# Kernel tuning notes

Hardware: AMD Instinct MI355X
Metric: run time of the kernel (lower is better)

## Reference

```python
import jax, jax.numpy as jnp
import numpy as np

N, TX, TZ, DX, DZ, DATT, DOUT = 8, 2048, 2048, 1024, 1024, 1024, 1024


def setup_inputs() -> dict:
    key = jax.random.key(0)
    ks = jax.random.split(key, 8)
    s = 0.02
    x = jax.random.normal(ks[0], (N, TX, DX), dtype=jnp.float32)
    z = jax.random.normal(ks[1], (N, TZ, DZ), dtype=jnp.float32)
    Wq = jax.random.normal(ks[2], (DX, DATT), dtype=jnp.float32) * s
    bq = jnp.zeros((DATT,), dtype=jnp.float32)
    Wk = jax.random.normal(ks[3], (DZ, DATT), dtype=jnp.float32) * s
    bk = jnp.zeros((DATT,), dtype=jnp.float32)
    Wv = jax.random.normal(ks[4], (DZ, DOUT), dtype=jnp.float32) * s
    bv = jnp.zeros((DOUT,), dtype=jnp.float32)
    # fixed boolean mask [Tx, Tz]; causal lower-triangular so no row is fully masked
    mask = jnp.tril(jnp.ones((TX, TZ), dtype=bool))
    return {"x": x, "z": z, "Wq": Wq, "bq": bq, "Wk": Wk, "bk": bk,
            "Wv": Wv, "bv": bv, "mask": mask}


def reference(x, z, Wq, bq, Wk, bk, Wv, bv, mask):
    Datt = Wq.shape[1]
    Q = x @ Wq + bq                      # [N, Tx, Datt]
    K = z @ Wk + bk                      # [N, Tz, Datt]
    V = z @ Wv + bv                      # [N, Tz, Dout]
    S = jnp.einsum('bxd,bzd->bxz', Q, K)  # [N, Tx, Tz]
    S = jnp.where(mask[None, :, :], S, -jnp.inf)
    A = jax.nn.softmax(S / jnp.sqrt(jnp.float32(Datt)), axis=-1)
    y = jnp.einsum('bxz,bzo->bxo', A, V)  # [N, Tx, Dout]
    return y
```

## Files before the change

### kernel.cpp

```cpp
#include <hip/hip_runtime.h>

typedef _Float16 f16;
typedef _Float16 f16x8 __attribute__((ext_vector_type(8)));
typedef _Float16 f16x4 __attribute__((ext_vector_type(4)));
typedef float    f32x4 __attribute__((ext_vector_type(4)));

constexpr int NB   = 8;
constexpr int T    = 2048;
constexpr int D    = 1024;
constexpr int NTRI = 136;

__device__ __forceinline__ void load_lds16(const f16* g, f16* l) {
    __builtin_amdgcn_global_load_lds(
        (const __attribute__((address_space(1))) void*)g,
        (__attribute__((address_space(3))) void*)l, 16, 0, 0);
}

__global__ __launch_bounds__(256) void cast_transpose_w(
    const float* __restrict__ W0, const float* __restrict__ W1,
    const float* __restrict__ W2, f16* __restrict__ Wt)
{
    __shared__ f16 tile[32][33];
    const int which = blockIdx.z;
    const float* W = which == 0 ? W0 : (which == 1 ? W1 : W2);
    f16* dst = Wt + (size_t)which * D * D;
    const int c0 = blockIdx.x * 32, r0 = blockIdx.y * 32;
    const int tx = threadIdx.x & 31, ty = threadIdx.x >> 5;
    #pragma unroll
    for (int i = 0; i < 32; i += 8)
        tile[ty + i][tx] = (f16)W[(size_t)(r0 + ty + i) * D + c0 + tx];
    __syncthreads();
    #pragma unroll
    for (int i = 0; i < 32; i += 8)
        dst[(size_t)(c0 + ty + i) * D + r0 + tx] = tile[tx][ty + i];
}

__global__ __launch_bounds__(256) void cast_xz(
    const float* __restrict__ x, const float* __restrict__ z,
    f16* __restrict__ xh, f16* __restrict__ zh)
{
    const float* src = blockIdx.y ? z : x;
    f16* dst = blockIdx.y ? zh : xh;
    const size_t i = ((size_t)blockIdx.x * 256 + threadIdx.x) * 4;
    const float4 v = *(const float4*)(src + i);
    f16x4 u = { (f16)v.x, (f16)v.y, (f16)v.z, (f16)v.w };
    *(f16x4*)(dst + i) = u;
}

template<int MODE>
__global__ __launch_bounds__(256) void gemm_nt(
    const f16* __restrict__ Ag_, const f16* __restrict__ Bg_,
    void* __restrict__ Cg_, void* __restrict__ Cg2_,
    const float* __restrict__ bias, const float* __restrict__ bias2,
    float* __restrict__ rsum)
{
    __shared__ f16 As[2 * 128 * 32];
    __shared__ f16 Bs[2 * 128 * 32];

    int bx, by;
    const int bz = blockIdx.z;
    if (MODE == 1) {
        const int idx = blockIdx.x;
        by = (int)((sqrtf(8.0f * idx + 1.0f) - 1.0f) * 0.5f);
        while ((by + 1) * (by + 2) / 2 <= idx) ++by;
        while (by * (by + 1) / 2 > idx) --by;
        bx = idx - by * (by + 1) / 2;
    } else if (MODE == 2) {
        bx = blockIdx.x; by = 15 - blockIdx.y;
    } else {
        bx = blockIdx.x; by = blockIdx.y;
    }

    const size_t bm0 = (size_t)by * 128, bn0 = (size_t)bx * 128;
    const f16* Abase; const f16* Bbase;
    int lda, ldb, K;
    if (MODE == 0 || MODE == 4) {
        Abase = Ag_ + bm0 * D;                       lda = D;
        Bbase = Bg_ + bn0 * D;                       ldb = D; K = D;
    } else if (MODE == 1) {
        Abase = Ag_ + (size_t)bz * T * D + bm0 * D;  lda = D;
        Bbase = Bg_ + (size_t)bz * T * D + bn0 * D;  ldb = D; K = D;
    } else {
        Abase = Ag_ + ((size_t)bz * NTRI + (size_t)by * (by + 1) / 2) * 16384;
        lda = 128;
        Bbase = Bg_ + (size_t)bz * D * T + bn0 * T;  ldb = T;
        K = (by + 1) * 128;
    }

    const int t    = threadIdx.x;
    const int lane = t & 63, wave = t >> 6;
    const int wr   = (wave >> 1) * 64, wc = (wave & 1) * 64;
    const int fr   = lane & 15, fo = (lane >> 4) * 8;
    const int srow = t >> 2;
    const int scol = (t & 3) * 8;
    const int wub  = (t & 192) * 8;

    f32x4 acc[4][4] = {};

    for (int k0 = 0; k0 < K; k0 += 64) {
        #pragma unroll
        for (int p = 0; p < 2; ++p) {
            const int k = k0 + p * 32;
            const f16* Ak;
            if (MODE == 2) Ak = Abase + (size_t)(k >> 7) * 16384 + (k & 127);
            else           Ak = Abase + k;
            #pragma unroll
            for (int it = 0; it < 2; ++it)
                load_lds16(Ak + (size_t)(it * 64 + srow) * lda + scol,
                           As + p * 4096 + it * 2048 + wub);
            #pragma unroll
            for (int it = 0; it < 2; ++it)
                load_lds16(Bbase + k + (size_t)(it * 64 + srow) * ldb + scol,
                           Bs + p * 4096 + it * 2048 + wub);
        }
        __syncthreads();

        #pragma unroll
        for (int p = 0; p < 2; ++p) {
            f16x8 av[4], bv[4];
            #pragma unroll
            for (int i = 0; i < 4; ++i)
                av[i] = *(const f16x8*)&As[p * 4096 + (wr + i * 16 + fr) * 32 + fo];
            #pragma unroll
            for (int j = 0; j < 4; ++j)
                bv[j] = *(const f16x8*)&Bs[p * 4096 + (wc + j * 16 + fr) * 32 + fo];
            #pragma unroll
            for (int i = 0; i < 4; ++i)
                #pragma unroll
                for (int j = 0; j < 4; ++j)
                    acc[i][j] = __builtin_amdgcn_mfma_f32_16x16x32_f16(av[i], bv[j], acc[i][j], 0, 0, 0);
        }
        __syncthreads();
    }

    const int cr = (lane >> 4) * 4, cc = lane & 15;
    if (MODE == 0) {
        f16* Cp = (f16*)Cg_;
        #pragma unroll
        for (int j = 0; j < 4; ++j) {
            const int col = (int)bn0 + wc + j * 16 + cc;
            const float bb = bias[col];
            #pragma unroll
            for (int i = 0; i < 4; ++i)
                #pragma unroll
                for (int g = 0; g < 4; ++g)
                    Cp[(bm0 + wr + i * 16 + cr + g) * D + col] = (f16)(acc[i][j][g] + bb);
        }
    } else if (MODE == 4) {
        if (bx < 8) {
            f16* Cp = (f16*)Cg_;
            #pragma unroll
            for (int j = 0; j < 4; ++j) {
                const int col = (int)bn0 + wc + j * 16 + cc;
                const float bb = bias[col];
                #pragma unroll
                for (int i = 0; i < 4; ++i)
                    #pragma unroll
                    for (int g = 0; g < 4; ++g)
                        Cp[(bm0 + wr + i * 16 + cr + g) * D + col] = (f16)(acc[i][j][g] + bb);
            }
        } else {
            f16* Vt = (f16*)Cg2_;
            const int b  = (int)(bm0 >> 11);
            const int r0 = (int)(bm0 & 2047);
            #pragma unroll
            for (int j = 0; j < 4; ++j) {
                const int colv = (int)bn0 - 1024 + wc + j * 16 + cc;
                const float bb = bias2[colv];
                #pragma unroll
                for (int i = 0; i < 4; ++i) {
                    f16x4 pk = { (f16)(acc[i][j][0] + bb), (f16)(acc[i][j][1] + bb),
                                 (f16)(acc[i][j][2] + bb), (f16)(acc[i][j][3] + bb) };
                    *(f16x4*)&Vt[(size_t)b * D * T + (size_t)colv * T + r0 + wr + i * 16 + cr] = pk;
                }
            }
        }
    } else if (MODE == 1) {
        f16* Cp = (f16*)Cg_ + ((size_t)bz * NTRI + (size_t)by * (by + 1) / 2 + bx) * 16384;
        float* rs = rsum + (size_t)bz * T + bm0;
        float rowsum[4][4] = {};
        #pragma unroll
        for (int i = 0; i < 4; ++i)
            #pragma unroll
            for (int j = 0; j < 4; ++j)
                #pragma unroll
                for (int g = 0; g < 4; ++g) {
                    const int lr = wr + i * 16 + cr + g, lc = wc + j * 16 + cc;
                    const int r = (int)bm0 + lr, c = (int)bn0 + lc;
                    const float p = (c > r) ? 0.0f : __expf(acc[i][j][g] * 0.03125f);
                    Cp[lr * 128 + lc] = (f16)p;
                    rowsum[i][g] += p;
                }
        #pragma unroll
        for (int i = 0; i < 4; ++i)
            #pragma unroll
            for (int g = 0; g < 4; ++g) {
                float s = rowsum[i][g];
                s += __shfl_xor(s, 1, 64);
                s += __shfl_xor(s, 2, 64);
                s += __shfl_xor(s, 4, 64);
                s += __shfl_xor(s, 8, 64);
                if (cc == 0) atomicAdd(&rs[wr + i * 16 + cr + g], s);
            }
    } else {
        float* Cp = (float*)Cg_ + (size_t)bz * T * D;
        const float* rs = rsum + (size_t)bz * T;
        #pragma unroll
        for (int i = 0; i < 4; ++i) {
            const int r4 = (int)bm0 + wr + i * 16 + cr;
            float rinv[4];
            #pragma unroll
            for (int g = 0; g < 4; ++g) rinv[g] = 1.0f / rs[r4 + g];
            #pragma unroll
            for (int j = 0; j < 4; ++j)
                #pragma unroll
                for (int g = 0; g < 4; ++g)
                    Cp[(size_t)(r4 + g) * D + bn0 + wc + j * 16 + cc] = acc[i][j][g] * rinv[g];
        }
    }
}

extern "C" void kernel_launch(void* const* d_in, const int* in_sizes, int n_in,
                              void* d_out, int out_size, void* d_ws, size_t ws_size,
                              hipStream_t stream)
{
    const float* x  = (const float*)d_in[0];
    const float* z  = (const float*)d_in[1];
    const float* Wq = (const float*)d_in[2];
    const float* bq = (const float*)d_in[3];
    const float* Wk = (const float*)d_in[4];
    const float* bk = (const float*)d_in[5];
    const float* Wv = (const float*)d_in[6];
    const float* bv = (const float*)d_in[7];
    float* out = (float*)d_out;

    char* ws = (char*)d_ws;
    f16*   Wt   = (f16*)(ws);
    f16*   xh   = (f16*)(ws + 6291456ull);
    f16*   zh   = (f16*)(ws + 39845888ull);
    f16*   Qh   = (f16*)(ws + 73400320ull);
    f16*   Kh   = (f16*)(ws + 106954752ull);
    f16*   Vt   = (f16*)(ws + 140509184ull);
    f16*   SA   = (f16*)(ws + 174063616ull);
    float* rsum = (float*)(ws + 209715200ull);

    hipMemsetAsync(rsum, 0, (size_t)NB * T * sizeof(float), stream);
    cast_transpose_w<<<dim3(32, 32, 3), 256, 0, stream>>>(Wq, Wk, Wv, Wt);
    cast_xz<<<dim3(16384, 2, 1), 256, 0, stream>>>(x, z, xh, zh);
    gemm_nt<0><<<dim3(8, 128, 1), 256, 0, stream>>>(xh, Wt, Qh, nullptr, bq, nullptr, nullptr);
    gemm_nt<4><<<dim3(16, 128, 1), 256, 0, stream>>>(zh, Wt + 1048576, Kh, Vt, bk, bv, nullptr);
    gemm_nt<1><<<dim3(136, 1, 8), 256, 0, stream>>>(Qh, Kh, SA, nullptr, nullptr, nullptr, rsum);
    gemm_nt<2><<<dim3(8, 16, 8), 256, 0, stream>>>(SA, Vt, out, nullptr, nullptr, nullptr, rsum);
}
```

Before: 500.2 us.

## Fuse fp32-to-fp16 input cast into a single QKV projection GEMM

Removes the separate cast_xz kernel and the fp16 copies of x and z. A new gemm_qkv kernel loads fp32 x/z tiles straight into XOR-swizzled LDS and converts them to fp16 in registers before the MFMA, which saves a full read-write pass over the activations. It also merges the Q and K/V projection launches into one 24-column grid. The attention GEMMs drop from a 64-wide double-buffered K step to a 32-wide single buffer, which halves LDS use but doubles the number of barriers. The cast now uses round-toward-zero, a small change in numerics.

```diff
diff --git a/kernel.cpp b/kernel.cpp
--- a/kernel.cpp
+++ b/kernel.cpp
@@ -3,6 +3,7 @@
 typedef _Float16 f16;
 typedef _Float16 f16x8 __attribute__((ext_vector_type(8)));
 typedef _Float16 f16x4 __attribute__((ext_vector_type(4)));
+typedef __fp16   h16x2 __attribute__((ext_vector_type(2)));
 typedef float    f32x4 __attribute__((ext_vector_type(4)));
 
 constexpr int NB   = 8;
@@ -10,7 +11,7 @@
 constexpr int D    = 1024;
 constexpr int NTRI = 136;
 
-__device__ __forceinline__ void load_lds16(const f16* g, f16* l) {
+__device__ __forceinline__ void load_lds16(const void* g, void* l) {
     __builtin_amdgcn_global_load_lds(
         (const __attribute__((address_space(1))) void*)g,
         (__attribute__((address_space(3))) void*)l, 16, 0, 0);
@@ -35,27 +36,107 @@
         dst[(size_t)(c0 + ty + i) * D + r0 + tx] = tile[tx][ty + i];
 }
 
-__global__ __launch_bounds__(256) void cast_xz(
-    const float* __restrict__ x, const float* __restrict__ z,
-    f16* __restrict__ xh, f16* __restrict__ zh)
-{
-    const float* src = blockIdx.y ? z : x;
-    f16* dst = blockIdx.y ? zh : xh;
-    const size_t i = ((size_t)blockIdx.x * 256 + threadIdx.x) * 4;
-    const float4 v = *(const float4*)(src + i);
-    f16x4 u = { (f16)v.x, (f16)v.y, (f16)v.z, (f16)v.w };
-    *(f16x4*)(dst + i) = u;
+__global__ __launch_bounds__(256) void gemm_qkv(
+    const float* __restrict__ xg, const float* __restrict__ zg,
+    const f16* __restrict__ Wt,
+    f16* __restrict__ Qh, f16* __restrict__ Kh, f16* __restrict__ Vt,
+    const float* __restrict__ bq, const float* __restrict__ bk,
+    const float* __restrict__ bv)
+{
+    __shared__ __align__(16) float As32[128 * 32];
+    __shared__ __align__(16) f16   Bs[128 * 32];
+
+    const int bx = blockIdx.x, by = blockIdx.y;
+    const size_t bm0 = (size_t)by * 128, bn0 = (size_t)bx * 128;
+    const float* Ag = (bx < 8) ? xg : zg;
+    const f16*   Bg = Wt + bn0 * D;
+
+    const int t    = threadIdx.x;
+    const int lane = t & 63, wave = t >> 6;
+    const int wr   = (wave >> 1) * 64, wc = (wave & 1) * 64;
+    const int fr   = lane & 15, fo = (lane >> 4) * 8;
+    const int srow16 = t >> 2, scol16 = (t & 3) * 8, wub16 = (t & 192) * 8;
+    const int arow = (lane >> 3);
+    const int acol = (((lane & 7) ^ arow) << 2);
+
+    f32x4 acc[4][4] = {};
+
+    for (int k0 = 0; k0 < D; k0 += 32) {
+        #pragma unroll
+        for (int it = 0; it < 4; ++it)
+            load_lds16(Ag + (bm0 + it * 32 + wave * 8 + arow) * D + k0 + acol,
+                       As32 + it * 1024 + wave * 256);
+        #pragma unroll
+        for (int it = 0; it < 2; ++it)
+            load_lds16(Bg + k0 + (size_t)(it * 64 + srow16) * D + scol16,
+                       Bs + it * 2048 + wub16);
+        __syncthreads();
+
+        f16x8 av[4], bvv[4];
+        #pragma unroll
+        for (int i = 0; i < 4; ++i) {
+            const int rA = wr + i * 16 + fr;
+            const int sw = rA & 7;
+            const float* Ra = As32 + rA * 32;
+            const float4 lo = *(const float4*)(Ra + ((((fo >> 2) + 0) ^ sw) << 2));
+            const float4 hi = *(const float4*)(Ra + ((((fo >> 2) + 1) ^ sw) << 2));
+            union { f16x8 v; h16x2 h[4]; } u;
+            u.h[0] = __builtin_amdgcn_cvt_pkrtz(lo.x, lo.y);
+            u.h[1] = __builtin_amdgcn_cvt_pkrtz(lo.z, lo.w);
+            u.h[2] = __builtin_amdgcn_cvt_pkrtz(hi.x, hi.y);
+            u.h[3] = __builtin_amdgcn_cvt_pkrtz(hi.z, hi.w);
+            av[i] = u.v;
+        }
+        #pragma unroll
+        for (int j = 0; j < 4; ++j)
+            bvv[j] = *(const f16x8*)&Bs[(wc + j * 16 + fr) * 32 + fo];
+        #pragma unroll
+        for (int i = 0; i < 4; ++i)
+            #pragma unroll
+            for (int j = 0; j < 4; ++j)
+                acc[i][j] = __builtin_amdgcn_mfma_f32_16x16x32_f16(av[i], bvv[j], acc[i][j], 0, 0, 0);
+        __syncthreads();
+    }
+
+    const int cr = (lane >> 4) * 4, cc = lane & 15;
+    const int grp = bx >> 3;
+    if (grp < 2) {
+        f16* Cp = grp == 0 ? Qh : Kh;
+        const float* bias = grp == 0 ? bq : bk;
+        #pragma unroll
+        for (int j = 0; j < 4; ++j) {
+            const int col = (int)bn0 - grp * 1024 + wc + j * 16 + cc;
+            const float bb = bias[col];
+            #pragma unroll
+            for (int i = 0; i < 4; ++i)
+                #pragma unroll
+                for (int g = 0; g < 4; ++g)
+                    Cp[(bm0 + wr + i * 16 + cr + g) * D + col] = (f16)(acc[i][j][g] + bb);
+        }
+    } else {
+        const int b  = (int)(bm0 >> 11);
+        const int r0 = (int)(bm0 & 2047);
+        #pragma unroll
+        for (int j = 0; j < 4; ++j) {
+            const int colv = (int)bn0 - 2048 + wc + j * 16 + cc;
+            const float bb = bv[colv];
+            #pragma unroll
+            for (int i = 0; i < 4; ++i) {
+                f16x4 pk = { (f16)(acc[i][j][0] + bb), (f16)(acc[i][j][1] + bb),
+                             (f16)(acc[i][j][2] + bb), (f16)(acc[i][j][3] + bb) };
+                *(f16x4*)&Vt[(size_t)b * D * T + (size_t)colv * T + r0 + wr + i * 16 + cr] = pk;
+            }
+        }
+    }
 }
 
 template<int MODE>
-__global__ __launch_bounds__(256) void gemm_nt(
+__global__ __launch_bounds__(256) void gemm_attn(
     const f16* __restrict__ Ag_, const f16* __restrict__ Bg_,
-    void* __restrict__ Cg_, void* __restrict__ Cg2_,
-    const float* __restrict__ bias, const float* __restrict__ bias2,
-    float* __restrict__ rsum)
-{
-    __shared__ f16 As[2 * 128 * 32];
-    __shared__ f16 Bs[2 * 128 * 32];
+    void* __restrict__ Cg_, float* __restrict__ rsum)
+{
+    __shared__ __align__(16) f16 As[128 * 32];
+    __shared__ __align__(16) f16 Bs[128 * 32];
 
     int bx, by;
     const int bz = blockIdx.z;
@@ -65,19 +146,14 @@
         while ((by + 1) * (by + 2) / 2 <= idx) ++by;
         while (by * (by + 1) / 2 > idx) --by;
         bx = idx - by * (by + 1) / 2;
-    } else if (MODE == 2) {
+    } else {
         bx = blockIdx.x; by = 15 - blockIdx.y;
-    } else {
-        bx = blockIdx.x; by = blockIdx.y;
     }
 
     const size_t bm0 = (size_t)by * 128, bn0 = (size_t)bx * 128;
     const f16* Abase; const f16* Bbase;
     int lda, ldb, K;
-    if (MODE == 0 || MODE == 4) {
-        Abase = Ag_ + bm0 * D;                       lda = D;
-        Bbase = Bg_ + bn0 * D;                       ldb = D; K = D;
-    } else if (MODE == 1) {
+    if (MODE == 1) {
         Abase = Ag_ + (size_t)bz * T * D + bm0 * D;  lda = D;
         Bbase = Bg_ + (size_t)bz * T * D + bn0 * D;  ldb = D; K = D;
     } else {
@@ -91,91 +167,41 @@
     const int lane = t & 63, wave = t >> 6;
     const int wr   = (wave >> 1) * 64, wc = (wave & 1) * 64;
     const int fr   = lane & 15, fo = (lane >> 4) * 8;
-    const int srow = t >> 2;
-    const int scol = (t & 3) * 8;
-    const int wub  = (t & 192) * 8;
+    const int srow = t >> 2, scol = (t & 3) * 8, wub = (t & 192) * 8;
 
     f32x4 acc[4][4] = {};
 
-    for (int k0 = 0; k0 < K; k0 += 64) {
-        #pragma unroll
-        for (int p = 0; p < 2; ++p) {
-            const int k = k0 + p * 32;
-            const f16* Ak;
-            if (MODE == 2) Ak = Abase + (size_t)(k >> 7) * 16384 + (k & 127);
-            else           Ak = Abase + k;
-            #pragma unroll
-            for (int it = 0; it < 2; ++it)
-                load_lds16(Ak + (size_t)(it * 64 + srow) * lda + scol,
-                           As + p * 4096 + it * 2048 + wub);
-            #pragma unroll
-            for (int it = 0; it < 2; ++it)
-                load_lds16(Bbase + k + (size_t)(it * 64 + srow) * ldb + scol,
-                           Bs + p * 4096 + it * 2048 + wub);
-        }
-        __syncthreads();
-
-        #pragma unroll
-        for (int p = 0; p < 2; ++p) {
-            f16x8 av[4], bv[4];
-            #pragma unroll
-            for (int i = 0; i < 4; ++i)
-                av[i] = *(const f16x8*)&As[p * 4096 + (wr + i * 16 + fr) * 32 + fo];
-            #pragma unroll
-            for (int j = 0; j < 4; ++j)
-                bv[j] = *(const f16x8*)&Bs[p * 4096 + (wc + j * 16 + fr) * 32 + fo];
-            #pragma unroll
-            for (int i = 0; i < 4; ++i)
-                #pragma unroll
-                for (int j = 0; j < 4; ++j)
-                    acc[i][j] = __builtin_amdgcn_mfma_f32_16x16x32_f16(av[i], bv[j], acc[i][j], 0, 0, 0);
-        }
+    for (int k0 = 0; k0 < K; k0 += 32) {
+        const f16* Ak;
+        if (MODE == 2) Ak = Abase + (size_t)(k0 >> 7) * 16384 + (k0 & 127);
+        else           Ak = Abase + k0;
+        #pragma unroll
+        for (int it = 0; it < 2; ++it)
+            load_lds16(Ak + (size_t)(it * 64 + srow) * lda + scol,
+                       As + it * 2048 + wub);
+        #pragma unroll
+        for (int it = 0; it < 2; ++it)
+            load_lds16(Bbase + k0 + (size_t)(it * 64 + srow) * ldb + scol,
+                       Bs + it * 2048 + wub);
+        __syncthreads();
+
+        f16x8 av[4], bvv[4];
+        #pragma unroll
+        for (int i = 0; i < 4; ++i)
+            av[i] = *(const f16x8*)&As[(wr + i * 16 + fr) * 32 + fo];
+        #pragma unroll
+        for (int j = 0; j < 4; ++j)
+            bvv[j] = *(const f16x8*)&Bs[(wc + j * 16 + fr) * 32 + fo];
+        #pragma unroll
+        for (int i = 0; i < 4; ++i)
+            #pragma unroll
+            for (int j = 0; j < 4; ++j)
+                acc[i][j] = __builtin_amdgcn_mfma_f32_16x16x32_f16(av[i], bvv[j], acc[i][j], 0, 0, 0);
         __syncthreads();
     }
 
     const int cr = (lane >> 4) * 4, cc = lane & 15;
-    if (MODE == 0) {
-        f16* Cp = (f16*)Cg_;
-        #pragma unroll
-        for (int j = 0; j < 4; ++j) {
-            const int col = (int)bn0 + wc + j * 16 + cc;
-            const float bb = bias[col];
-            #pragma unroll
-            for (int i = 0; i < 4; ++i)
-                #pragma unroll
-                for (int g = 0; g < 4; ++g)
-                    Cp[(bm0 + wr + i * 16 + cr + g) * D + col] = (f16)(acc[i][j][g] + bb);
-        }
-    } else if (MODE == 4) {
-        if (bx < 8) {
-            f16* Cp = (f16*)Cg_;
-            #pragma unroll
-            for (int j = 0; j < 4; ++j) {
-                const int col = (int)bn0 + wc + j * 16 + cc;
-                const float bb = bias[col];
-                #pragma unroll
-                for (int i = 0; i < 4; ++i)
-                    #pragma unroll
-                    for (int g = 0; g < 4; ++g)
-                        Cp[(bm0 + wr + i * 16 + cr + g) * D + col] = (f16)(acc[i][j][g] + bb);
-            }
-        } else {
-            f16* Vt = (f16*)Cg2_;
-            const int b  = (int)(bm0 >> 11);
-            const int r0 = (int)(bm0 & 2047);
-            #pragma unroll
-            for (int j = 0; j < 4; ++j) {
-                const int colv = (int)bn0 - 1024 + wc + j * 16 + cc;
-                const float bb = bias2[colv];
-                #pragma unroll
-                for (int i = 0; i < 4; ++i) {
-                    f16x4 pk = { (f16)(acc[i][j][0] + bb), (f16)(acc[i][j][1] + bb),
-                                 (f16)(acc[i][j][2] + bb), (f16)(acc[i][j][3] + bb) };
-                    *(f16x4*)&Vt[(size_t)b * D * T + (size_t)colv * T + r0 + wr + i * 16 + cr] = pk;
-                }
-            }
-        }
-    } else if (MODE == 1) {
+    if (MODE == 1) {
         f16* Cp = (f16*)Cg_ + ((size_t)bz * NTRI + (size_t)by * (by + 1) / 2 + bx) * 16384;
         float* rs = rsum + (size_t)bz * T + bm0;
         float rowsum[4][4] = {};
@@ -236,19 +262,15 @@
 
     char* ws = (char*)d_ws;
     f16*   Wt   = (f16*)(ws);
-    f16*   xh   = (f16*)(ws + 6291456ull);
-    f16*   zh   = (f16*)(ws + 39845888ull);
-    f16*   Qh   = (f16*)(ws + 73400320ull);
-    f16*   Kh   = (f16*)(ws + 106954752ull);
-    f16*   Vt   = (f16*)(ws + 140509184ull);
-    f16*   SA   = (f16*)(ws + 174063616ull);
-    float* rsum = (float*)(ws + 209715200ull);
-
-    hipMemsetAsync(rsum, 0, (size_t)NB * T * sizeof(float), stream);
+    f16*   Qh   = (f16*)(ws + 6291456ull);
+    f16*   Kh   = (f16*)(ws + 39845888ull);
+    f16*   Vt   = (f16*)(ws + 73400320ull);
+    f16*   SA   = (f16*)(ws + 106954752ull);
+    float* rsum = (float*)(ws + 142606336ull);
+
+    (void)hipMemsetAsync(rsum, 0, (size_t)NB * T * sizeof(float), stream);
     cast_transpose_w<<<dim3(32, 32, 3), 256, 0, stream>>>(Wq, Wk, Wv, Wt);
-    cast_xz<<<dim3(16384, 2, 1), 256, 0, stream>>>(x, z, xh, zh);
-    gemm_nt<0><<<dim3(8, 128, 1), 256, 0, stream>>>(xh, Wt, Qh, nullptr, bq, nullptr, nullptr);
-    gemm_nt<4><<<dim3(16, 128, 1), 256, 0, stream>>>(zh, Wt + 1048576, Kh, Vt, bk, bv, nullptr);
-    gemm_nt<1><<<dim3(136, 1, 8), 256, 0, stream>>>(Qh, Kh, SA, nullptr, nullptr, nullptr, rsum);
-    gemm_nt<2><<<dim3(8, 16, 8), 256, 0, stream>>>(SA, Vt, out, nullptr, nullptr, nullptr, rsum);
-}
+    gemm_qkv<<<dim3(24, 128, 1), 256, 0, stream>>>(x, z, Wt, Qh, Kh, Vt, bq, bk, bv);
+    gemm_attn<1><<<dim3(136, 1, 8), 256, 0, stream>>>(Qh, Kh, SA, rsum);
+    gemm_attn<2><<<dim3(8, 16, 8), 256, 0, stream>>>(SA, Vt, out, rsum);
+}
```

New measurement: 579.2 us. 1.16x slower.
